# Kernel tuning notes

Measured on AMD Instinct MI355X. Metric: run time of the kernel, lower is better.

## Reference

```python
import jax, jax.numpy as jnp
import numpy as np
from math import factorial as fact

L, P, T, CIN, COUT, N = 4, 5, 15, 32, 32, 1000


def _cg(j1, m1, j2, m2, J, M):
    # Clebsch-Gordan coefficient <j1 m1 j2 m2 | J M> (integer args, Racah formula)
    if m1 + m2 != M or not (abs(j1 - j2) <= J <= j1 + j2):
        return 0.0
    if abs(m1) > j1 or abs(m2) > j2 or abs(M) > J:
        return 0.0
    pre = (2.0 * J + 1.0) * fact(J + j1 - j2) * fact(J - j1 + j2) * fact(j1 + j2 - J) / fact(j1 + j2 + J + 1)
    pre *= fact(J + M) * fact(J - M) * fact(j1 - m1) * fact(j1 + m1) * fact(j2 - m2) * fact(j2 + m2)
    s = 0.0
    for k in range(0, j1 + j2 - J + 1):
        d = (k, j1 + j2 - J - k, j1 - m1 - k, j2 + m2 - k, J - j2 + m1 + k, J - j1 - m2 + k)
        if min(d) < 0:
            continue
        den = 1.0
        for x in d:
            den *= fact(x)
        s += (-1.0) ** k / den
    return float(np.sqrt(pre) * s)


def _precompute(Ldeg):
    # Mirrors PrecomputingTensorsForConv6D
    tensors, coefs = [], []
    for l in range(Ldeg):
        for l1 in range(Ldeg):
            for l2 in range(abs(l - l1), min(Ldeg, l + l1 + 1)):
                coefs.append(8.0 * np.pi ** 2 / (2 * l1 + 1)
                             * np.sqrt((2 * l + 1) * (2 * l1 + 1) / (4.0 * np.pi * (2 * l2 + 1)))
                             * _cg(l, 0, l1, 0, l2, 0))
                T1 = np.zeros((l + 1, l1 + 1, l2 + 1)); T2 = np.zeros_like(T1); T3 = np.zeros_like(T1)
                for k in range(l + 1):
                    for k1 in range(l1 + 1):
                        if abs(k + k1) < l2 + 1:
                            T1[k, k1, k + k1] = _cg(l, k, l1, k1, l2, k + k1) * (-1) ** k1
                        if k1 > 0 and abs(k - k1) < l2 + 1:
                            if k - k1 >= 0:
                                T2[k, k1, k - k1] = _cg(l, k, l1, -k1, l2, k - k1) * (-1) ** l1
                            else:
                                T3[k, k1, k1 - k] = (-1) ** (k1 - k) * (-1) ** (l1 + l2) * _cg(l, k, l1, -k1, l2, k - k1)
                tensors.append((jnp.asarray(T1, jnp.float32), jnp.asarray(T2, jnp.float32), jnp.asarray(T3, jnp.float32)))
    return tensors, np.asarray(coefs, np.float64)

_TENSORS, _COEFS = _precompute(L)


def setup_inputs() -> dict:
    key = jax.random.key(0)
    ks = iter(jax.random.split(key, 64))
    inp = {}
    for l in range(L):
        inp[f"in{l}_real"] = 0.1 * jax.random.normal(next(ks), (N, T, l + 1, P, CIN), jnp.float32)
        inp[f"in{l}_imag"] = 0.1 * jax.random.normal(next(ks), (N, T, l + 1, P, CIN), jnp.float32)
    for l in range(L):
        inp[f"w{l}_real"] = 0.05 * jax.random.normal(next(ks), (l + 1, T, P, CIN, COUT), jnp.float32)
        inp[f"w{l}_imag"] = 0.05 * jax.random.normal(next(ks), (l + 1, T, P, CIN, COUT), jnp.float32)
    for l in range(L):
        inp[f"b{l}_real"] = jax.random.uniform(next(ks), (1, l + 1, P, COUT), jnp.float32, -0.05, 0.05)
        inp[f"b{l}_imag"] = jax.random.uniform(next(ks), (1, l + 1, P, COUT), jnp.float32, -0.05, 0.05)
    return inp


def _forward(ins, ws_raw, bs_raw):
    # Mask imaginary parts: weight order-0 row (k=0) and bias degree-0 component are zeroed,
    # exactly as the temp_term masks in build().
    ws, bs = [], []
    for l in range(L):
        wmask = jnp.ones((l + 1, 1, 1, 1, 1), jnp.float32).at[0].set(0.0)
        ws += [ws_raw[2 * l], ws_raw[2 * l + 1] * wmask]
        bmask = jnp.ones((1, l + 1, 1, 1), jnp.float32).at[:, 0].set(0.0)
        bs += [bs_raw[2 * l], bs_raw[2 * l + 1] * bmask]
    outputs = []
    itr = 0
    for l in range(L):
        out_r = 0.0
        out_i = 0.0
        for l1 in range(L):
            for l2 in range(abs(l - l1), min(L, l + l1 + 1)):
                c = float(_COEFS[itr])
                T1, T2, T3 = _TENSORS[itr]
                xr, xi = ins[2 * l2], ins[2 * l2 + 1]      # [N, T, l2+1, P, Cin]
                wr, wi = ws[2 * l1], ws[2 * l1 + 1]        # [l1+1, T, P, Cin, Cout]
                # complex CG contraction -> [N, l+1, P, Cout]
                out_r = out_r + c * jnp.einsum('lmk,ntkpi,mtpij->nlpj', T1 + T2 + T3, xr, wr)
                out_r = out_r - c * jnp.einsum('lmk,ntkpi,mtpij->nlpj', T1 - T2 + T3, xi, wi)
                out_i = out_i + c * jnp.einsum('lmk,ntkpi,mtpij->nlpj', T1 - T2 - T3, xr, wi)
                out_i = out_i + c * jnp.einsum('lmk,ntkpi,mtpij->nlpj', T1 + T2 - T3, xi, wr)
                itr += 1
        outputs.append(out_r + bs[2 * l])
        outputs.append(out_i + bs[2 * l + 1])
    return tuple(outputs)


def reference(in0_real, in0_imag, in1_real, in1_imag, in2_real, in2_imag, in3_real, in3_imag,
              w0_real, w0_imag, w1_real, w1_imag, w2_real, w2_imag, w3_real, w3_imag,
              b0_real, b0_imag, b1_real, b1_imag, b2_real, b2_imag, b3_real, b3_imag):
    ins = [in0_real, in0_imag, in1_real, in1_imag, in2_real, in2_imag, in3_real, in3_imag]
    ws = [w0_real, w0_imag, w1_real, w1_imag, w2_real, w2_imag, w3_real, w3_imag]
    bs = [b0_real, b0_imag, b1_real, b1_imag, b2_real, b2_imag, b3_real, b3_imag]
    return _forward(ins, ws, bs)
```

## Files before the change

kernel.cpp:

```cpp
#include <hip/hip_runtime.h>
#include <hip/hip_bf16.h>

#define NB   1000
#define NPAD 1024
#define TT   15
#define PP   5
#define CI   32
#define CO   32
#define KDIM 9600
#define MDIM 640
#define NCHUNK 300
#define NCOL   20
#define TABN  16384
#define KSTEPS 150
#define WTELEMS 1536000
#define XCVT_BLOCKS 6000
#define WTRX_BLOCKS 300
#define TAB_BLOCKS (TABN / 256)

typedef __attribute__((ext_vector_type(8))) short          bf16x8;
typedef __attribute__((ext_vector_type(8))) unsigned short ushort8;
typedef __attribute__((ext_vector_type(4))) float          f32x4;

struct Chunks {
  short ci[NCHUNK]; short l2[NCHUNK]; short t[NCHUNK]; short k2[NCHUNK];
  short xidx[NCHUNK]; short cls[NCHUNK]; int ns[NCHUNK]; int offc[NCHUNK];
};
constexpr Chunks mkchunks() {
  Chunks c{};
  int idx = 0;
  for (int l2 = 0; l2 < 4; ++l2)
    for (int ci = 0; ci < 2; ++ci)
      for (int t = 0; t < TT; ++t)
        for (int k2 = 0; k2 <= l2; ++k2) {
          c.ci[idx] = (short)ci; c.l2[idx] = (short)l2;
          c.t[idx] = (short)t;   c.k2[idx] = (short)k2;
          c.xidx[idx] = (short)(2 * l2 + ci);
          c.cls[idx]  = (short)(l2 * (l2 + 1) / 2 + k2);
          c.ns[idx]   = TT * (l2 + 1) * PP * CI;
          c.offc[idx] = (t * (l2 + 1) + k2) * PP * CI;
          ++idx;
        }
  return c;
}
__constant__ Chunks g_ck = mkchunks();

struct Cols { int l[NCOL]; int lm[NCOL]; int ci[NCOL]; long obase[NCOL]; };
constexpr Cols mkcols() {
  Cols c{};
  long acc = 0; int idx = 0;
  for (int l = 0; l < 4; ++l)
    for (int ci = 0; ci < 2; ++ci) {
      for (int lm = 0; lm <= l; ++lm) {
        c.l[idx] = l; c.lm[idx] = lm; c.ci[idx] = ci; c.obase[idx] = acc; ++idx;
      }
      acc += (long)NB * (l + 1) * PP * CO;
    }
  return c;
}
__constant__ Cols g_cols = mkcols();

constexpr int wtsize(int tensor) { return ((tensor >> 1) + 1) * TT * PP * CI * CO; }
struct WOffs { int off[8]; int sz[8]; };
constexpr WOffs mkwoffs() {
  WOffs w{}; int acc = 0;
  for (int i = 0; i < 8; ++i) { w.off[i] = acc; w.sz[i] = wtsize(i); acc += w.sz[i]; }
  return w;
}
__constant__ WOffs g_wo = mkwoffs();

__constant__ short g_l1of[10] = {0,1,1,2,2,2,3,3,3,3};
__constant__ short g_mof[10]  = {0,0,1,0,1,2,0,1,2,3};
__constant__ short g_wtT[20] = {0,1,2,2,3,3,4,4,4,5,5,5,6,6,6,6,7,7,7,7};
__constant__ short g_wtM[20] = {0,0,0,1,0,1,0,1,2,0,1,2,0,1,2,3,0,1,2,3};

__device__ double dfact(int n) { double r = 1.0; for (int i = 2; i <= n; ++i) r *= i; return r; }

__device__ double dcg(int j1, int m1, int j2, int m2, int J, int M) {
  if (m1 + m2 != M) return 0.0;
  int lo = j1 - j2; if (lo < 0) lo = -lo;
  if (J < lo || J > j1 + j2) return 0.0;
  int am1 = m1 < 0 ? -m1 : m1, am2 = m2 < 0 ? -m2 : m2, aM = M < 0 ? -M : M;
  if (am1 > j1 || am2 > j2 || aM > J) return 0.0;
  double pre = (2.0 * J + 1.0) * dfact(J + j1 - j2) * dfact(J - j1 + j2) * dfact(j1 + j2 - J)
               / dfact(j1 + j2 + J + 1);
  pre *= dfact(J + M) * dfact(J - M) * dfact(j1 - m1) * dfact(j1 + m1) * dfact(j2 - m2) * dfact(j2 + m2);
  double s = 0.0;
  for (int k = 0; k <= j1 + j2 - J; ++k) {
    int d1 = j1 + j2 - J - k, d2 = j1 - m1 - k, d3 = j2 + m2 - k,
        d4 = J - j2 + m1 + k, d5 = J - j1 - m2 + k;
    if (d1 < 0 || d2 < 0 || d3 < 0 || d4 < 0 || d5 < 0) continue;
    double den = dfact(k) * dfact(d1) * dfact(d2) * dfact(d3) * dfact(d4) * dfact(d5);
    s += ((k & 1) ? -1.0 : 1.0) / den;
  }
  return sqrt(pre) * s;
}

struct PArgs { const float* w[8]; const float* x[8]; float* wt; float* tab; unsigned short* xb; };

__global__ __launch_bounds__(256) void k_prep(PArgs A) {
  const int bx = blockIdx.x, tid = threadIdx.x;
  __shared__ float lds[5][32][33];

  if (bx < XCVT_BLOCKS) {
    int g = bx * 256 + tid;
    int chunk = g % 300;
    int rest = g / 300;
    int n = rest & (NPAD - 1);
    int p = rest >> 10;
    ushort8* dst = (ushort8*)(A.xb + ((size_t)(p * NPAD + n)) * KDIM + chunk * 32);
    if (n < NB) {
      const float* xp = A.x[g_ck.xidx[chunk]] + (size_t)n * g_ck.ns[chunk]
                        + g_ck.offc[chunk] + p * CI;
      float4 v[8];
      #pragma unroll
      for (int e = 0; e < 8; ++e) v[e] = *(const float4*)(xp + 4 * e);
      #pragma unroll
      for (int q = 0; q < 4; ++q) {
        float4 a = v[2 * q], b = v[2 * q + 1];
        float fa[8] = {a.x, a.y, a.z, a.w, b.x, b.y, b.z, b.w};
        ushort8 o;
        #pragma unroll
        for (int e = 0; e < 8; ++e) {
          unsigned u = __float_as_uint(fa[e]);
          u += 0x7fff + ((u >> 16) & 1);
          o[e] = (unsigned short)(u >> 16);
        }
        dst[q] = o;
      }
    } else {
      ushort8 z = {0,0,0,0,0,0,0,0};
      #pragma unroll
      for (int q = 0; q < 4; ++q) dst[q] = z;
    }
  } else if (bx < XCVT_BLOCKS + WTRX_BLOCKS) {
    int b = bx - XCVT_BLOCKS;
    int t_ = b % TT;
    int mrow = b / TT;
    int tensor = g_wtT[mrow], m = g_wtM[mrow];
    const float* src = A.w[tensor] + (size_t)(m * TT + t_) * (PP * CI * CO);
    #pragma unroll
    for (int k = 0; k < 5; ++k) {
      int f = tid + k * 256;
      float4 v = *(const float4*)(src + f * 4);
      int elem = f * 4;
      int p = elem >> 10, rem = elem & 1023;
      int i = rem >> 5, j0 = rem & 31;
      lds[p][i][j0] = v.x; lds[p][i][j0 + 1] = v.y;
      lds[p][i][j0 + 2] = v.z; lds[p][i][j0 + 3] = v.w;
    }
    __syncthreads();
    float* dst = A.wt + g_wo.off[tensor] + (size_t)m * (PP * CO * TT * CI) + t_ * CI;
    #pragma unroll
    for (int k = 0; k < 20; ++k) {
      int e = tid + k * 256;
      int i = e & 31, pj = e >> 5;
      dst[pj * (TT * CI) + i] = lds[pj >> 5][i][pj & 31];
    }
  } else {
    int idx = (bx - XCVT_BLOCKS - WTRX_BLOCKS) * 256 + tid;
    int k2 = idx & 3, m = (idx >> 2) & 3, lm = (idx >> 4) & 3, l2 = (idx >> 6) & 3,
        l1 = (idx >> 8) & 3, l = (idx >> 10) & 3, combo = (idx >> 12) & 3;
    float v = 0.f;
    int dlo = l - l1; if (dlo < 0) dlo = -dlo;
    bool valid = (lm <= l) && (m <= l1) && (k2 <= l2) && (l2 >= dlo) && (l2 <= l + l1);
    if (valid) {
      const double PI = 3.14159265358979323846;
      double coef = 8.0 * PI * PI / (2.0 * l1 + 1.0)
                    * sqrt((2.0 * l + 1.0) * (2.0 * l1 + 1.0) / (4.0 * PI * (2.0 * l2 + 1.0)))
                    * dcg(l, 0, l1, 0, l2, 0);
      double t1 = 0.0, t2 = 0.0, t3 = 0.0;
      if (k2 == lm + m)
        t1 = dcg(l, lm, l1, m, l2, k2) * ((m & 1) ? -1.0 : 1.0);
      if (m > 0 && lm - m >= 0 && k2 == lm - m)
        t2 = dcg(l, lm, l1, -m, l2, lm - m) * ((l1 & 1) ? -1.0 : 1.0);
      if (m > 0 && lm - m < 0 && k2 == m - lm)
        t3 = (((m - lm) & 1) ? -1.0 : 1.0) * (((l1 + l2) & 1) ? -1.0 : 1.0)
             * dcg(l, lm, l1, -m, l2, lm - m);
      double r = 0.0;
      if (combo == 0) r =  coef * (t1 + t2 + t3);
      else if (combo == 1) r = -coef * (t1 - t2 + t3);
      else if (combo == 2) r =  coef * (t1 - t2 - t3);
      else r = coef * (t1 + t2 - t3);
      v = (float)r;
    }
    A.tab[idx] = v;
  }
}

struct FArgs { const float* wt; const float* tab; unsigned short* weffT; };

__global__ __launch_bounds__(256) void k_fold(FArgs A) {
  const int tid = threadIdx.x;
  const int mo = blockIdx.x, p = blockIdx.y;
  const int j = mo & 31, col = mo >> 5;
  const int l = g_cols.l[col], lm = g_cols.lm[col], cio = g_cols.ci[col];
  __shared__ float ldsW[2][10][480];
  __shared__ float ldsC[2][10][10];

  for (int e = tid; e < 2 * 10 * 480; e += 256) {
    int ti = e % 480;
    int rowid = e / 480;
    int wci = rowid / 10, r = rowid % 10;
    int l1 = g_l1of[r], m = g_mof[r];
    ldsW[wci][r][ti] = A.wt[g_wo.off[2 * l1 + wci] + m * (PP * CO * TT * CI)
                            + (p * CO + j) * (TT * CI) + ti];
  }
  if (tid < 200) {
    int r = tid % 10, clk = (tid / 10) % 10, ci = tid / 100;
    int l1 = g_l1of[r], m = g_mof[r];
    int l2 = g_l1of[clk], k2 = g_mof[clk];
    int combo = cio * 2 + ci, wci = cio ^ ci;
    float v = 0.f;
    int dlo = l - l1; if (dlo < 0) dlo = -dlo;
    if (l2 >= dlo && l2 <= l + l1 && m <= l1 && k2 <= l2)
      v = A.tab[(((((combo * 4 + l) * 4 + l1) * 4 + l2) * 4 + lm) * 4 + m) * 4 + k2];
    if (wci == 1 && m == 0) v = 0.f;
    ldsC[ci][clk][r] = v;
  }
  __syncthreads();

  unsigned short* dst = A.weffT + ((size_t)(p * MDIM + mo)) * KDIM;
  for (int kk = tid; kk < KDIM; kk += 256) {
    int chunk = kk >> 5, i = kk & 31;
    int ci = g_ck.ci[chunk], t = g_ck.t[chunk], cls = g_ck.cls[chunk];
    int wci = cio ^ ci;
    float s = 0.f;
    #pragma unroll
    for (int r = 0; r < 10; ++r)
      s += ldsC[ci][cls][r] * ldsW[wci][r][t * 32 + i];
    unsigned u = __float_as_uint(s);
    u += 0x7fff + ((u >> 16) & 1);
    dst[kk] = (unsigned short)(u >> 16);
  }
}

__device__ __forceinline__ void gl_lds16(const void* g, void* l) {
  __builtin_amdgcn_global_load_lds(
      (const __attribute__((address_space(1))) unsigned int*)g,
      (__attribute__((address_space(3))) unsigned int*)l, 16, 0, 0);
}

struct GArgs { const unsigned short* xb; const unsigned short* weffT; float* partial; int nsplit; };

__global__ __launch_bounds__(256, 4) void k_gemm(GArgs A) {
  const int tid = threadIdx.x;
  const int lane = tid & 63;
  const int wv = tid >> 6, wr = wv >> 1, wc = wv & 1;
  const int NS = A.nsplit;

  const int x = blockIdx.x & 7;
  const int jj = blockIdx.x >> 3;
  const int perx = 25 * NS;
  const int full = perx / 40;
  int zz, slot;
  if (jj < full * 40) { zz = x + 8 * (jj / 40); slot = jj % 40; }
  else {
    int leftover = perx - full * 40;
    int idx = x * leftover + (jj - full * 40);
    zz = full * 8 + idx / 40; slot = idx % 40;
  }
  const int n0 = (slot & 7) * 128, mo0 = (slot >> 3) * 128;
  const int p = zz / NS, sp = zz % NS;
  const int bsteps = KSTEPS / NS, rem = KSTEPS % NS;
  const int mysteps = bsteps + (sp < rem ? 1 : 0);
  const int sstart = sp * bsteps + (sp < rem ? sp : rem);

  __shared__ __align__(16) unsigned short sA[128 * 64];
  __shared__ __align__(16) unsigned short sB[128 * 64];
  f32x4 acc[4][4] = {};

  int aoff[4];
  #pragma unroll
  for (int u = 0; u < 4; ++u) {
    int s = u * 256 + tid;
    int row = s >> 3;
    int qs = (s & 7) ^ (row & 7);
    aoff[u] = row * KDIM + qs * 8;
  }
  const unsigned short* xbase = A.xb + (size_t)p * NPAD * KDIM + (size_t)n0 * KDIM + sstart * 64;
  const unsigned short* wbase = A.weffT + (size_t)p * MDIM * KDIM + (size_t)mo0 * KDIM + sstart * 64;

  for (int cc = 0; cc < mysteps; ++cc) {
    const unsigned short* xs = xbase + cc * 64;
    const unsigned short* ws = wbase + cc * 64;
    #pragma unroll
    for (int u = 0; u < 4; ++u) {
      gl_lds16(xs + aoff[u], (void*)(sA + (u * 256 + tid) * 8));
      gl_lds16(ws + aoff[u], (void*)(sB + (u * 256 + tid) * 8));
    }
    __syncthreads();
    #pragma unroll
    for (int ks = 0; ks < 2; ++ks) {
      const int q = ks * 4 + (lane >> 4);
      bf16x8 af[4], bfr[4];
      #pragma unroll
      for (int m = 0; m < 4; ++m) {
        int ra = wr * 64 + m * 16 + (lane & 15);
        af[m] = *(const bf16x8*)(sA + ra * 64 + ((q ^ (ra & 7)) << 3));
      }
      #pragma unroll
      for (int n = 0; n < 4; ++n) {
        int rb = wc * 64 + n * 16 + (lane & 15);
        bfr[n] = *(const bf16x8*)(sB + rb * 64 + ((q ^ (rb & 7)) << 3));
      }
      #pragma unroll
      for (int m = 0; m < 4; ++m)
        #pragma unroll
        for (int n = 0; n < 4; ++n)
          acc[m][n] = __builtin_amdgcn_mfma_f32_16x16x32_bf16(af[m], bfr[n], acc[m][n], 0, 0, 0);
    }
    __syncthreads();
  }

  float* pout = A.partial + (size_t)zz * (NPAD * MDIM);
  #pragma unroll
  for (int m = 0; m < 4; ++m) {
    #pragma unroll
    for (int nn = 0; nn < 4; ++nn) {
      int mo = mo0 + wc * 64 + nn * 16 + (lane & 15);
      #pragma unroll
      for (int r = 0; r < 4; ++r) {
        int n = n0 + wr * 64 + m * 16 + (lane >> 4) * 4 + r;
        pout[(size_t)n * MDIM + mo] = acc[m][nn][r];
      }
    }
  }
}

struct RArgs { const float* partial; const float* b[8]; float* out; int nsplit; };

__global__ __launch_bounds__(256) void k_red(RArgs A) {
  int e4 = blockIdx.x * 256 + threadIdx.x;
  if (e4 >= NB * (MDIM / 4) * PP) return;
  int mo4 = e4 % (MDIM / 4);
  int rest = e4 / (MDIM / 4);
  int n = rest % NB;
  int p = rest / NB;
  int mo = mo4 * 4;
  float4 s = make_float4(0.f, 0.f, 0.f, 0.f);
  for (int sp = 0; sp < A.nsplit; ++sp) {
    float4 v = *(const float4*)&A.partial[((size_t)(p * A.nsplit + sp) * NPAD + n) * MDIM + mo];
    s.x += v.x; s.y += v.y; s.z += v.z; s.w += v.w;
  }
  int colid = mo >> 5, j = mo & 31;
  int l = g_cols.l[colid], lmv = g_cols.lm[colid], cio = g_cols.ci[colid];
  long base = g_cols.obase[colid];
  float4 bias = *(const float4*)&A.b[2 * l + cio][(lmv * PP + p) * CO + j];
  if (cio == 1 && lmv == 0) bias = make_float4(0.f, 0.f, 0.f, 0.f);
  float4 o = make_float4(s.x + bias.x, s.y + bias.y, s.z + bias.z, s.w + bias.w);
  *(float4*)&A.out[base + (((size_t)n * (l + 1) + lmv) * PP + p) * CO + j] = o;
}

extern "C" void kernel_launch(void* const* d_in, const int* in_sizes, int n_in,
                              void* d_out, int out_size, void* d_ws, size_t ws_size,
                              hipStream_t stream) {
  float* tab = (float*)d_ws;
  float* wt  = tab + TABN;
  unsigned short* weffT = (unsigned short*)(wt + WTELEMS);
  unsigned short* xb    = weffT + (size_t)PP * MDIM * KDIM;
  float* partial = (float*)(xb + (size_t)PP * NPAD * KDIM);

  size_t base_bytes = (size_t)TABN * 4 + (size_t)WTELEMS * 4
                    + (size_t)PP * MDIM * KDIM * 2 + (size_t)PP * NPAD * KDIM * 2;
  size_t per_split = (size_t)PP * NPAD * MDIM * 4;
  int NS = 1;
  for (int c = 5; c >= 2; --c)
    if (ws_size >= base_bytes + (size_t)c * per_split) { NS = c; break; }

  PArgs pa;
  for (int i = 0; i < 8; ++i) pa.w[i] = (const float*)d_in[8 + i];
  for (int i = 0; i < 8; ++i) pa.x[i] = (const float*)d_in[i];
  pa.wt = wt; pa.tab = tab; pa.xb = xb;
  k_prep<<<dim3(XCVT_BLOCKS + WTRX_BLOCKS + TAB_BLOCKS), dim3(256), 0, stream>>>(pa);

  FArgs fa;
  fa.wt = wt; fa.tab = (const float*)tab; fa.weffT = weffT;
  k_fold<<<dim3(MDIM, PP), dim3(256), 0, stream>>>(fa);

  GArgs ga;
  ga.xb = xb; ga.weffT = weffT; ga.partial = partial; ga.nsplit = NS;
  k_gemm<<<dim3(200 * NS), dim3(256), 0, stream>>>(ga);

  RArgs ra;
  ra.partial = partial; ra.out = (float*)d_out; ra.nsplit = NS;
  for (int i = 0; i < 8; ++i) ra.b[i] = (const float*)d_in[16 + i];
  k_red<<<dim3((NB * (MDIM / 4) * PP + 255) / 256), dim3(256), 0, stream>>>(ra);
}
```

Baseline: 236.4 us.

## Double-buffer LDS tiles with K=32 steps to overlap global loads with MFMA

```diff
diff --git a/kernel.cpp b/kernel.cpp
--- a/kernel.cpp
+++ b/kernel.cpp
@@ -12,7 +12,7 @@
 #define NCHUNK 300
 #define NCOL   20
 #define TABN  16384
-#define KSTEPS 150
+#define KT32  300
 #define WTELEMS 1536000
 #define XCVT_BLOCKS 6000
 #define WTRX_BLOCKS 300
@@ -262,55 +262,79 @@
   }
   const int n0 = (slot & 7) * 128, mo0 = (slot >> 3) * 128;
   const int p = zz / NS, sp = zz % NS;
-  const int bsteps = KSTEPS / NS, rem = KSTEPS % NS;
+  const int bsteps = KT32 / NS, rem = KT32 % NS;
   const int mysteps = bsteps + (sp < rem ? 1 : 0);
   const int sstart = sp * bsteps + (sp < rem ? sp : rem);
 
-  __shared__ __align__(16) unsigned short sA[128 * 64];
-  __shared__ __align__(16) unsigned short sB[128 * 64];
+  __shared__ __align__(16) unsigned short sA[2 * 128 * 32];
+  __shared__ __align__(16) unsigned short sB[2 * 128 * 32];
   f32x4 acc[4][4] = {};
 
-  int aoff[4];
+  int aoff[2];
   #pragma unroll
-  for (int u = 0; u < 4; ++u) {
+  for (int u = 0; u < 2; ++u) {
     int s = u * 256 + tid;
-    int row = s >> 3;
-    int qs = (s & 7) ^ (row & 7);
+    int row = s >> 2;
+    int qs = (s & 3) ^ ((row >> 1) & 3);
     aoff[u] = row * KDIM + qs * 8;
   }
-  const unsigned short* xbase = A.xb + (size_t)p * NPAD * KDIM + (size_t)n0 * KDIM + sstart * 64;
-  const unsigned short* wbase = A.weffT + (size_t)p * MDIM * KDIM + (size_t)mo0 * KDIM + sstart * 64;
-
-  for (int cc = 0; cc < mysteps; ++cc) {
-    const unsigned short* xs = xbase + cc * 64;
-    const unsigned short* ws = wbase + cc * 64;
-    #pragma unroll
-    for (int u = 0; u < 4; ++u) {
-      gl_lds16(xs + aoff[u], (void*)(sA + (u * 256 + tid) * 8));
-      gl_lds16(ws + aoff[u], (void*)(sB + (u * 256 + tid) * 8));
-    }
-    __syncthreads();
-    #pragma unroll
-    for (int ks = 0; ks < 2; ++ks) {
-      const int q = ks * 4 + (lane >> 4);
-      bf16x8 af[4], bfr[4];
-      #pragma unroll
-      for (int m = 0; m < 4; ++m) {
-        int ra = wr * 64 + m * 16 + (lane & 15);
-        af[m] = *(const bf16x8*)(sA + ra * 64 + ((q ^ (ra & 7)) << 3));
-      }
-      #pragma unroll
-      for (int n = 0; n < 4; ++n) {
-        int rb = wc * 64 + n * 16 + (lane & 15);
-        bfr[n] = *(const bf16x8*)(sB + rb * 64 + ((q ^ (rb & 7)) << 3));
-      }
-      #pragma unroll
-      for (int m = 0; m < 4; ++m)
-        #pragma unroll
-        for (int n = 0; n < 4; ++n)
-          acc[m][n] = __builtin_amdgcn_mfma_f32_16x16x32_bf16(af[m], bfr[n], acc[m][n], 0, 0, 0);
-    }
-    __syncthreads();
+  const unsigned short* xbase = A.xb + (size_t)p * NPAD * KDIM + (size_t)n0 * KDIM + sstart * 32;
+  const unsigned short* wbase = A.weffT + (size_t)p * MDIM * KDIM + (size_t)mo0 * KDIM + sstart * 32;
+
+#define STAGE32(BUF, step) {                                                        \
+    const unsigned short* xs = xbase + (size_t)(step) * 32;                         \
+    const unsigned short* ws = wbase + (size_t)(step) * 32;                         \
+    unsigned short* la = sA + (BUF) * 4096;                                         \
+    unsigned short* lb = sB + (BUF) * 4096;                                         \
+    _Pragma("unroll")                                                               \
+    for (int u = 0; u < 2; ++u) {                                                   \
+      gl_lds16(xs + aoff[u], (void*)(la + (u * 256 + tid) * 8));                    \
+      gl_lds16(ws + aoff[u], (void*)(lb + (u * 256 + tid) * 8));                    \
+    } }
+
+#define COMPUTE32(BUF) {                                                            \
+    const unsigned short* la = sA + (BUF) * 4096;                                   \
+    const unsigned short* lb = sB + (BUF) * 4096;                                   \
+    const int q = lane >> 4;                                                        \
+    bf16x8 af[4], bfr[4];                                                           \
+    _Pragma("unroll")                                                               \
+    for (int m = 0; m < 4; ++m) {                                                   \
+      int ra = wr * 64 + m * 16 + (lane & 15);                                      \
+      af[m] = *(const bf16x8*)(la + ra * 32 + ((q ^ ((ra >> 1) & 3)) << 3));        \
+    }                                                                               \
+    _Pragma("unroll")                                                               \
+    for (int n = 0; n < 4; ++n) {                                                   \
+      int rb = wc * 64 + n * 16 + (lane & 15);                                      \
+      bfr[n] = *(const bf16x8*)(lb + rb * 32 + ((q ^ ((rb >> 1) & 3)) << 3));       \
+    }                                                                               \
+    _Pragma("unroll")                                                               \
+    for (int m = 0; m < 4; ++m)                                                     \
+      _Pragma("unroll")                                                             \
+      for (int n = 0; n < 4; ++n)                                                   \
+        acc[m][n] = __builtin_amdgcn_mfma_f32_16x16x32_bf16(af[m], bfr[n],          \
+                                                            acc[m][n], 0, 0, 0);    \
+  }
+
+#define ITER32(BUF) {                                                               \
+    if (t + 1 < mysteps) asm volatile("s_waitcnt vmcnt(4)" ::: "memory");           \
+    else                 asm volatile("s_waitcnt vmcnt(0)" ::: "memory");           \
+    __builtin_amdgcn_s_barrier();                                                   \
+    __builtin_amdgcn_sched_barrier(0);                                              \
+    COMPUTE32(BUF);                                                                 \
+    asm volatile("" ::: "memory");                                                  \
+    __builtin_amdgcn_s_barrier();                                                   \
+    asm volatile("" ::: "memory");                                                  \
+    if (t + 2 < mysteps) STAGE32(BUF, t + 2);                                       \
+  }
+
+  STAGE32(0, 0);
+  if (mysteps > 1) STAGE32(1, 1);
+  int t = 0;
+  while (t < mysteps) {
+    ITER32(0);
+    if (++t >= mysteps) break;
+    ITER32(1);
+    ++t;
   }
 
   float* pout = A.partial + (size_t)zz * (NPAD * MDIM);
@@ -326,6 +350,9 @@
       }
     }
   }
+#undef STAGE32
+#undef COMPUTE32
+#undef ITER32
 }
 
 struct RArgs { const float* partial; const float* b[8]; float* out; int nsplit; };
```

Result: slower. 447.3 us (+89.2%).
